# Performance work log

Measured on AMD Instinct MI355X. Metric: run time of the kernel, lower is better.

## Reference

```python
import jax, jax.numpy as jnp
import numpy as np

NPOINTS = 1024


def setup_inputs() -> dict:
    key = jax.random.key(0)
    B, N, C = 64, 131072, 3
    pos = jax.random.normal(key, (B, N, C), dtype=jnp.float32)
    return {"pos": pos, "start_idx": 0}


def reference(pos, start_idx):
    """Farthest point sampling. pos: (B, N, C) -> indices (B, NPOINTS) int32."""
    B, N, C = pos.shape
    start = jnp.full((B,), start_idx, dtype=jnp.int32)
    dist0 = jnp.full((B, N), jnp.inf, dtype=pos.dtype)

    def step(carry, _):
        dist, last = carry                                   # dist: (B,N), last: (B,)
        last_pos = jnp.take_along_axis(pos, last[:, None, None], axis=1)  # (B,1,C)
        d = jnp.sum((pos - last_pos) ** 2, axis=-1)          # (B,N) squared dist to newest sample
        dist = jnp.minimum(dist, d)                          # min to-sample-set distance
        nxt = jnp.argmax(dist, axis=-1).astype(jnp.int32)    # farthest point
        return (dist, nxt), last                             # emit index selected this step

    (_, _), idxs = jax.lax.scan(step, (dist0, start), None, length=NPOINTS)
    return idxs.T  # (B, NPOINTS); first column == start_idx
```

## Files before the change

### kernel.cpp

```cpp
#include <hip/hip_runtime.h>
#include <stdint.h>

#define NB    64
#define NN    131072
#define NPTS  1024
#define WPB   4
#define TPB   512
#define NWAVE (TPB / 64)
#define CHUNK (NN / WPB)
#define PPT   (CHUNK / TPB)
#define RPTS  38
#define LPTS  10
#define GPTS  16
#define RPAIR (RPTS / 2)
#define LPAIR (LPTS / 2)
#define GPAIR (GPTS / 2)

typedef float v2f __attribute__((ext_vector_type(2)));
typedef unsigned long long u64;


__global__ __launch_bounds__(TPB) void fps_kernel(
    const float* __restrict__ pos,
    const int*   __restrict__ start_p,
    int*         __restrict__ out,
    u64*         __restrict__ slots)
{
#pragma clang fp contract(off)
    const int wg   = blockIdx.x;
    const int xcd  = wg & 7;
    const int sl   = wg >> 3;
    const int b    = xcd * 8 + (sl >> 2);
    const int r    = sl & 3;
    const int t    = threadIdx.x;
    const int lane = t & 63;
    const int wv   = t >> 6;

    const float* __restrict__ P  = pos + (size_t)b * NN * 3;
    const float* __restrict__ Pc = P + (size_t)r * CHUNK * 3;
    u64* __restrict__ bslots = slots + (size_t)b * NPTS * WPB;

    __shared__ float ldsP[LPTS * TPB * 3];
    __shared__ u64   wred[2][NWAVE];

    v2f rx[RPAIR], ry[RPAIR], rz[RPAIR];
#pragma unroll
    for (int p = 0; p < RPAIR; ++p) {
        const float* a = Pc + (size_t)(t + (2 * p) * TPB) * 3;
        const float* c = a + (size_t)TPB * 3;
        rx[p] = (v2f){a[0], c[0]};
        ry[p] = (v2f){a[1], c[1]};
        rz[p] = (v2f){a[2], c[2]};
    }
#pragma unroll
    for (int j = 0; j < LPTS; ++j) {
        const float* a = Pc + (size_t)(t + (RPTS + j) * TPB) * 3;
        float* d = &ldsP[(size_t)(t + j * TPB) * 3];
        d[0] = a[0]; d[1] = a[1]; d[2] = a[2];
    }

    const int start = start_p[0];
    float sx = P[(size_t)start * 3 + 0];
    float sy = P[(size_t)start * 3 + 1];
    float sz = P[(size_t)start * 3 + 2];
    if (r == 0 && t == 0) out[(size_t)b * NPTS] = start;

    v2f dist[PPT / 2];
#pragma unroll
    for (int p = 0; p < PPT / 2; ++p)
        dist[p] = (v2f){__builtin_inff(), __builtin_inff()};

    const int gbase = r * CHUNK;

    for (int k = 1; k < NPTS; ++k) {
        const v2f s0 = (v2f){sx, sx}, s1 = (v2f){sy, sy}, s2 = (v2f){sz, sz};
        float best = -1.0f;
        int   bi   = 0;

        v2f gx[GPAIR], gy[GPAIR], gz[GPAIR];
#pragma unroll
        for (int p = 0; p < 4; ++p) {
            const float* a = Pc + (size_t)(t + (RPTS + LPTS + 2 * p) * TPB) * 3;
            const float* c = a + (size_t)TPB * 3;
            gx[p] = (v2f){a[0], c[0]};
            gy[p] = (v2f){a[1], c[1]};
            gz[p] = (v2f){a[2], c[2]};
        }

#define PAIR_STEP(DP, PX, PY, PZ, I0)                                    \
        {                                                                \
            v2f dx = (PX) - s0, dy = (PY) - s1, dz = (PZ) - s2;          \
            v2f d  = (dx * dx + dy * dy) + dz * dz;                      \
            v2f nd;                                                      \
            nd.x = fminf(dist[DP].x, d.x);                               \
            nd.y = fminf(dist[DP].y, d.y);                               \
            dist[DP] = nd;                                               \
            if (nd.x > best) { best = nd.x; bi = (I0); }                 \
            if (nd.y > best) { best = nd.y; bi = (I0) + TPB; }           \
        }

#pragma unroll
        for (int p = 0; p < RPAIR; ++p)
            PAIR_STEP(p, rx[p], ry[p], rz[p], gbase + t + (2 * p) * TPB);

#pragma unroll
        for (int p = 4; p < GPAIR; ++p) {
            const float* a = Pc + (size_t)(t + (RPTS + LPTS + 2 * p) * TPB) * 3;
            const float* c = a + (size_t)TPB * 3;
            gx[p] = (v2f){a[0], c[0]};
            gy[p] = (v2f){a[1], c[1]};
            gz[p] = (v2f){a[2], c[2]};
        }

#pragma unroll
        for (int p = 0; p < LPAIR; ++p) {
            const int li0 = (t + (2 * p) * TPB) * 3;
            const int li1 = li0 + TPB * 3;
            v2f px = (v2f){ldsP[li0 + 0], ldsP[li1 + 0]};
            v2f py = (v2f){ldsP[li0 + 1], ldsP[li1 + 1]};
            v2f pz = (v2f){ldsP[li0 + 2], ldsP[li1 + 2]};
            PAIR_STEP(RPAIR + p, px, py, pz, gbase + t + (RPTS + 2 * p) * TPB);
        }
#pragma unroll
        for (int p = 0; p < GPAIR; ++p)
            PAIR_STEP(RPAIR + LPAIR + p, gx[p], gy[p], gz[p],
                      gbase + t + (RPTS + LPTS + 2 * p) * TPB);
#undef PAIR_STEP

        u64 pk = ((u64)__float_as_uint(best) << 32) | (unsigned)~bi;

#pragma unroll
        for (int o = 32; o >= 1; o >>= 1) {
            u64 q = __shfl_xor(pk, o, 64);
            if (q > pk) pk = q;
        }
        if (lane == 0) wred[k & 1][wv] = pk;
        __syncthreads();

        u64 v = wred[k & 1][lane & (NWAVE - 1)];
#pragma unroll
        for (int o = 1; o < NWAVE; o <<= 1) {
            u64 q = __shfl_xor(v, o, 64);
            if (q > v) v = q;
        }
        if (t == 0)
            __hip_atomic_store(&bslots[(size_t)k * WPB + r], v,
                               __ATOMIC_RELAXED, __HIP_MEMORY_SCOPE_AGENT);

        const u64* sp = &bslots[(size_t)k * WPB + (lane & (WPB - 1))];
        u64 g;
        for (;;) {
            g = __hip_atomic_load(sp, __ATOMIC_RELAXED, __HIP_MEMORY_SCOPE_AGENT);
            if (g) break;
            __builtin_amdgcn_s_sleep(1);
        }
#pragma unroll
        for (int o = 1; o < WPB; o <<= 1) {
            u64 q = __shfl_xor(g, o, 64);
            if (q > g) g = q;
        }
        const int widx = (int)~(unsigned)g;
        if (r == 0 && t == 0) out[(size_t)b * NPTS + k] = widx;
        sx = P[(size_t)widx * 3 + 0];
        sy = P[(size_t)widx * 3 + 1];
        sz = P[(size_t)widx * 3 + 2];
    }
}

extern "C" void kernel_launch(void* const* d_in, const int* in_sizes, int n_in,
                              void* d_out, int out_size, void* d_ws, size_t ws_size,
                              hipStream_t stream)
{
    const float* pos     = (const float*)d_in[0];
    const int*   start_p = (const int*)d_in[1];
    int*         out     = (int*)d_out;
    u64*         slots   = (u64*)d_ws;

    hipMemsetAsync(d_ws, 0, (size_t)NB * NPTS * WPB * sizeof(u64), stream);

    void* args[] = { (void*)&pos, (void*)&start_p, (void*)&out, (void*)&slots };
    hipError_t e = hipLaunchCooperativeKernel((const void*)fps_kernel,
                                              dim3(NB * WPB), dim3(TPB),
                                              args, 0, stream);
    if (e != hipSuccess) {
        fps_kernel<<<dim3(NB * WPB), dim3(TPB), 0, stream>>>(pos, start_p, out, slots);
    }
}
```

Baseline: 4.410 ms.

## Double block size and keep all points in registers and SoA LDS

Doubles threads per block to 1024, so each thread owns 32 points instead of 64. 20 of them stay in registers and 12 sit in shared memory stored as separate x/y/z arrays with paired (vector) loads. This removes the per-iteration global reloads of 16 points per thread, and the per-lane fmin is replaced with an elementwise vector min. The cost is a larger in-block reduction across 16 waves and higher register pressure, capped by the waves_per_eu attribute.

After: 4.274 ms. 3.1% less time.

```diff
diff --git a/kernel.cpp b/kernel.cpp
--- a/kernel.cpp
+++ b/kernel.cpp
@@ -5,22 +5,30 @@
 #define NN    131072
 #define NPTS  1024
 #define WPB   4
-#define TPB   512
+#define TPB   1024
 #define NWAVE (TPB / 64)
 #define CHUNK (NN / WPB)
 #define PPT   (CHUNK / TPB)
-#define RPTS  38
-#define LPTS  10
-#define GPTS  16
+#define RPTS  20
+#define LPTS  12
 #define RPAIR (RPTS / 2)
 #define LPAIR (LPTS / 2)
-#define GPAIR (GPTS / 2)
 
 typedef float v2f __attribute__((ext_vector_type(2)));
 typedef unsigned long long u64;
 
+static __device__ __forceinline__ v2f vmin2(v2f a, v2f b) {
+#if __has_builtin(__builtin_elementwise_min)
+    return __builtin_elementwise_min(a, b);
+#else
+    v2f r; r.x = fminf(a.x, b.x); r.y = fminf(a.y, b.y); return r;
+#endif
+}
 
-__global__ __launch_bounds__(TPB) void fps_kernel(
+
+__global__ __launch_bounds__(TPB)
+__attribute__((amdgpu_waves_per_eu(4, 4)))
+void fps_kernel(
     const float* __restrict__ pos,
     const int*   __restrict__ start_p,
     int*         __restrict__ out,
@@ -40,7 +48,9 @@
     const float* __restrict__ Pc = P + (size_t)r * CHUNK * 3;
     u64* __restrict__ bslots = slots + (size_t)b * NPTS * WPB;
 
-    __shared__ float ldsP[LPTS * TPB * 3];
+    __shared__ float lx[LPAIR * TPB * 2];
+    __shared__ float ly[LPAIR * TPB * 2];
+    __shared__ float lz[LPAIR * TPB * 2];
     __shared__ u64   wred[2][NWAVE];
 
     v2f rx[RPAIR], ry[RPAIR], rz[RPAIR];
@@ -53,10 +63,13 @@
         rz[p] = (v2f){a[2], c[2]};
     }
 #pragma unroll
-    for (int j = 0; j < LPTS; ++j) {
-        const float* a = Pc + (size_t)(t + (RPTS + j) * TPB) * 3;
-        float* d = &ldsP[(size_t)(t + j * TPB) * 3];
-        d[0] = a[0]; d[1] = a[1]; d[2] = a[2];
+    for (int l = 0; l < LPAIR; ++l) {
+        const float* a = Pc + (size_t)(t + (RPTS + 2 * l) * TPB) * 3;
+        const float* c = a + (size_t)TPB * 3;
+        const int idx = (l * TPB + t) * 2;
+        lx[idx] = a[0]; lx[idx + 1] = c[0];
+        ly[idx] = a[1]; ly[idx + 1] = c[1];
+        lz[idx] = a[2]; lz[idx + 1] = c[2];
     }
 
     const int start = start_p[0];
@@ -73,27 +86,16 @@
     const int gbase = r * CHUNK;
 
     for (int k = 1; k < NPTS; ++k) {
+        const int bank = k & 1;
         const v2f s0 = (v2f){sx, sx}, s1 = (v2f){sy, sy}, s2 = (v2f){sz, sz};
         float best = -1.0f;
         int   bi   = 0;
-
-        v2f gx[GPAIR], gy[GPAIR], gz[GPAIR];
-#pragma unroll
-        for (int p = 0; p < 4; ++p) {
-            const float* a = Pc + (size_t)(t + (RPTS + LPTS + 2 * p) * TPB) * 3;
-            const float* c = a + (size_t)TPB * 3;
-            gx[p] = (v2f){a[0], c[0]};
-            gy[p] = (v2f){a[1], c[1]};
-            gz[p] = (v2f){a[2], c[2]};
-        }
 
 #define PAIR_STEP(DP, PX, PY, PZ, I0)                                    \
         {                                                                \
             v2f dx = (PX) - s0, dy = (PY) - s1, dz = (PZ) - s2;          \
             v2f d  = (dx * dx + dy * dy) + dz * dz;                      \
-            v2f nd;                                                      \
-            nd.x = fminf(dist[DP].x, d.x);                               \
-            nd.y = fminf(dist[DP].y, d.y);                               \
+            v2f nd = vmin2(dist[DP], d);                                 \
             dist[DP] = nd;                                               \
             if (nd.x > best) { best = nd.x; bi = (I0); }                 \
             if (nd.y > best) { best = nd.y; bi = (I0) + TPB; }           \
@@ -102,29 +104,14 @@
 #pragma unroll
         for (int p = 0; p < RPAIR; ++p)
             PAIR_STEP(p, rx[p], ry[p], rz[p], gbase + t + (2 * p) * TPB);
-
 #pragma unroll
-        for (int p = 4; p < GPAIR; ++p) {
-            const float* a = Pc + (size_t)(t + (RPTS + LPTS + 2 * p) * TPB) * 3;
-            const float* c = a + (size_t)TPB * 3;
-            gx[p] = (v2f){a[0], c[0]};
-            gy[p] = (v2f){a[1], c[1]};
-            gz[p] = (v2f){a[2], c[2]};
+        for (int l = 0; l < LPAIR; ++l) {
+            const int idx = (l * TPB + t) * 2;
+            v2f px = *reinterpret_cast<const v2f*>(&lx[idx]);
+            v2f py = *reinterpret_cast<const v2f*>(&ly[idx]);
+            v2f pz = *reinterpret_cast<const v2f*>(&lz[idx]);
+            PAIR_STEP(RPAIR + l, px, py, pz, gbase + t + (RPTS + 2 * l) * TPB);
         }
-
-#pragma unroll
-        for (int p = 0; p < LPAIR; ++p) {
-            const int li0 = (t + (2 * p) * TPB) * 3;
-            const int li1 = li0 + TPB * 3;
-            v2f px = (v2f){ldsP[li0 + 0], ldsP[li1 + 0]};
-            v2f py = (v2f){ldsP[li0 + 1], ldsP[li1 + 1]};
-            v2f pz = (v2f){ldsP[li0 + 2], ldsP[li1 + 2]};
-            PAIR_STEP(RPAIR + p, px, py, pz, gbase + t + (RPTS + 2 * p) * TPB);
-        }
-#pragma unroll
-        for (int p = 0; p < GPAIR; ++p)
-            PAIR_STEP(RPAIR + LPAIR + p, gx[p], gy[p], gz[p],
-                      gbase + t + (RPTS + LPTS + 2 * p) * TPB);
 #undef PAIR_STEP
 
         u64 pk = ((u64)__float_as_uint(best) << 32) | (unsigned)~bi;
@@ -134,10 +121,10 @@
             u64 q = __shfl_xor(pk, o, 64);
             if (q > pk) pk = q;
         }
-        if (lane == 0) wred[k & 1][wv] = pk;
+        if (lane == 0) wred[bank][wv] = pk;
         __syncthreads();
 
-        u64 v = wred[k & 1][lane & (NWAVE - 1)];
+        u64 v = wred[bank][lane & (NWAVE - 1)];
 #pragma unroll
         for (int o = 1; o < NWAVE; o <<= 1) {
             u64 q = __shfl_xor(v, o, 64);
@@ -147,7 +134,7 @@
             __hip_atomic_store(&bslots[(size_t)k * WPB + r], v,
                                __ATOMIC_RELAXED, __HIP_MEMORY_SCOPE_AGENT);
 
-        const u64* sp = &bslots[(size_t)k * WPB + (lane & (WPB - 1))];
+        const u64* sp = &bslots[(size_t)k * WPB + (lane & 3)];
         u64 g;
         for (;;) {
             g = __hip_atomic_load(sp, __ATOMIC_RELAXED, __HIP_MEMORY_SCOPE_AGENT);
@@ -155,7 +142,7 @@
             __builtin_amdgcn_s_sleep(1);
         }
 #pragma unroll
-        for (int o = 1; o < WPB; o <<= 1) {
+        for (int o = 1; o <= 2; o <<= 1) {
             u64 q = __shfl_xor(g, o, 64);
             if (q > g) g = q;
         }
```
